# Optimization experiments

Measured on AMD Instinct MI355X. Metric: run time of the kernel, lower is better.

The kernel has to match this reference:

```python
import jax, jax.numpy as jnp
import numpy as np
from jax import lax

N_LAYER = 4
D_MODEL = 512
N_HEAD = 8
D_HEAD = 64
D_INNER = 2048
KERNEL = 9
POOL = 8
N_CLASSES = 10
BATCH = 4
RAW_LEN = 8192


def setup_inputs() -> dict:
    key = jax.random.key(0)
    ks = jax.random.split(key, 12)
    s = 0.02
    return {
        "signal": jax.random.normal(ks[0], (BATCH, RAW_LEN), jnp.float32),
        "conv_w": jax.random.normal(ks[1], (KERNEL, 1, D_MODEL), jnp.float32) * s,
        "conv_b": jnp.zeros((D_MODEL,), jnp.float32),
        "qkv_w": jax.random.normal(ks[2], (N_LAYER, D_MODEL, 3 * N_HEAD * D_HEAD), jnp.float32) * s,
        "r_w": jax.random.normal(ks[3], (N_LAYER, D_MODEL, N_HEAD * D_HEAD), jnp.float32) * s,
        "o_w": jax.random.normal(ks[4], (N_LAYER, N_HEAD * D_HEAD, D_MODEL), jnp.float32) * s,
        "ff1_w": jax.random.normal(ks[5], (N_LAYER, D_MODEL, D_INNER), jnp.float32) * s,
        "ff1_b": jnp.zeros((N_LAYER, D_INNER), jnp.float32),
        "ff2_w": jax.random.normal(ks[6], (N_LAYER, D_INNER, D_MODEL), jnp.float32) * s,
        "ff2_b": jnp.zeros((N_LAYER, D_MODEL), jnp.float32),
        "r_w_bias": jax.random.normal(ks[7], (N_HEAD, D_HEAD), jnp.float32) * s,
        "r_r_bias": jax.random.normal(ks[8], (N_HEAD, D_HEAD), jnp.float32) * s,
        "fc_w": jax.random.normal(ks[9], (D_MODEL, N_CLASSES), jnp.float32) * s,
        "fc_b": jnp.zeros((N_CLASSES,), jnp.float32),
    }


def _rel_shift(x):
    # x: [qlen, rlen, bsz, n_head]; TF-XL pad/reshape/slice trick
    q, r, b, n = x.shape
    x = jnp.pad(x, ((0, 0), (1, 0), (0, 0), (0, 0)))
    x = x.reshape(r + 1, q, b, n)[1:]
    return x.reshape(q, r, b, n)


def _forward(signal, conv_w, conv_b, qkv_w, r_w, o_w, ff1_w, ff1_b, ff2_w,
             ff2_b, r_w_bias, r_r_bias, fc_w, fc_b):
    # Conv1D (valid) -> ReLU -> AveragePooling1D
    x = signal[:, :, None]  # [B, L, 1]
    x = lax.conv_general_dilated(x, conv_w, (1,), 'VALID',
                                 dimension_numbers=('NWC', 'WIO', 'NWC')) + conv_b
    x = jax.nn.relu(x)
    B, Lp, D = x.shape
    S = Lp // POOL  # Lp is divisible by POOL for our sizes (keras valid pooling)
    x = x[:, :S * POOL].reshape(B, S, POOL, D).mean(axis=2)
    core = x.transpose(1, 0, 2)  # [S, B, D]

    # sinusoidal relative positional embedding, pos_seq = S-1 .. -(S-1)
    pos_seq = jnp.arange(S - 1, -S, -1, dtype=core.dtype)  # [2S-1]
    inv_freq = 1.0 / (10000.0 ** (jnp.arange(0, D, 2, dtype=core.dtype) / D))
    sin_inp = pos_seq[:, None] * inv_freq[None, :]
    pos_emb = jnp.concatenate([jnp.sin(sin_inp), jnp.cos(sin_inp)], -1)  # [2S-1, D]

    scale = 1.0 / np.sqrt(D_HEAD).astype(np.float32)
    for l in range(N_LAYER):
        heads = core @ qkv_w[l]  # [S, B, 3*H*Dh]
        q, k, v = jnp.split(heads, 3, axis=-1)
        q = q.reshape(S, B, N_HEAD, D_HEAD)
        k = k.reshape(S, B, N_HEAD, D_HEAD)
        v = v.reshape(S, B, N_HEAD, D_HEAD)
        rk = (pos_emb @ r_w[l]).reshape(2 * S - 1, N_HEAD, D_HEAD)

        AC = jnp.einsum('ibnd,jbnd->ijbn', q + r_w_bias, k)      # content term
        BD = jnp.einsum('ibnd,jnd->ijbn', q + r_r_bias, rk)      # position term
        BD = _rel_shift(BD)[:, :S]                                # [S, S, B, H]
        attn_prob = jax.nn.softmax((AC + BD) * scale, axis=1)
        attn_vec = jnp.einsum('ijbn,jbnd->ibnd', attn_prob, v)
        attn_out = attn_vec.reshape(S, B, N_HEAD * D_HEAD) @ o_w[l]
        core = core + attn_out

        # position-wise FF with residual
        h = jax.nn.relu(core @ ff1_w[l] + ff1_b[l]) @ ff2_w[l] + ff2_b[l]
        core = core + h

    # classification head on last timestep
    return core[-1] @ fc_w + fc_b  # [B, n_classes]


def reference(signal, conv_w, conv_b, qkv_w, r_w, o_w, ff1_w, ff1_b, ff2_w,
              ff2_b, r_w_bias, r_r_bias, fc_w, fc_b):
    return _forward(signal, conv_w, conv_b, qkv_w, r_w, o_w, ff1_w, ff1_b,
                    ff2_w, ff2_b, r_w_bias, r_r_bias, fc_w, fc_b)
```

## Files before the change

kernel.cpp:

```cpp
#include <hip/hip_runtime.h>
#include <math.h>

#define S_LEN   1023
#define BATCH_N 4
#define DMODEL  512
#define NHEAD   8
#define DHEAD   64
#define DINNER  2048
#define NLAYER  4
#define RAWLEN  8192
#define POOLW   8
#define KERNW   9
#define RLEN    (2*S_LEN-1)
#define MROWS   (S_LEN*BATCH_N)

using bf16x8 = __attribute__((ext_vector_type(8))) short;
using f32x4  = __attribute__((ext_vector_type(4))) float;

__device__ __forceinline__ unsigned short f2bf(float f) {
    union { float f; unsigned int u; } v; v.f = f;
    unsigned int u = v.u;
    return (unsigned short)((u + 0x7fffu + ((u >> 16) & 1u)) >> 16);
}
__device__ __forceinline__ float bf2f(unsigned short h) {
    union { unsigned int u; float f; } v; v.u = ((unsigned int)h) << 16;
    return v.f;
}

__device__ __forceinline__ void gload_lds16(const void* g, void* l) {
    using gvoid = const __attribute__((address_space(1))) void;
    using lvoid = __attribute__((address_space(3))) void;
    gvoid* gp = reinterpret_cast<gvoid*>(reinterpret_cast<unsigned long long>(g));
    lvoid* lp = reinterpret_cast<lvoid*>((unsigned int)reinterpret_cast<unsigned long long>(l));
    __builtin_amdgcn_global_load_lds(gp, lp, 16, 0, 0);
}

__global__ __launch_bounds__(512) void conv_pool_kernel(
    const float* __restrict__ sig, const float* __restrict__ cw,
    const float* __restrict__ cb, float* __restrict__ core,
    unsigned short* __restrict__ core_bf)
{
    int s = blockIdx.x, b = blockIdx.y, d = threadIdx.x;
    __shared__ float sseg[POOLW + KERNW - 1];
    if (d < POOLW + KERNW - 1) sseg[d] = sig[b*RAWLEN + s*POOLW + d];
    __syncthreads();
    float w[KERNW];
#pragma unroll
    for (int k = 0; k < KERNW; k++) w[k] = cw[k*DMODEL + d];
    float bias = cb[d];
    float acc = 0.f;
#pragma unroll
    for (int p = 0; p < POOLW; p++) {
        float c = bias;
#pragma unroll
        for (int k = 0; k < KERNW; k++) c = fmaf(sseg[p+k], w[k], c);
        acc += fmaxf(c, 0.f);
    }
    float v = acc * (1.0f/POOLW);
    core[(s*BATCH_N + b)*DMODEL + d] = v;
    core_bf[(s*BATCH_N + b)*DMODEL + d] = f2bf(v);
}

__global__ __launch_bounds__(512) void posemb_kernel(unsigned short* __restrict__ pe)
{
    int j = blockIdx.x, d = threadIdx.x;
    float pos = (float)(S_LEN - 1 - j);
    int i = (d < 256) ? d : d - 256;
    float invf = exp2f(-(float)i * (13.287712f/256.0f));
    float a = pos * invf;
    pe[j*DMODEL + d] = f2bf((d < 256) ? __sinf(a) : __cosf(a));
}

__global__ __launch_bounds__(256) void transpose_all_kernel(
    const float* __restrict__ qw, const float* __restrict__ rw,
    const float* __restrict__ ow, const float* __restrict__ f1,
    const float* __restrict__ f2,
    unsigned short* __restrict__ qT, unsigned short* __restrict__ rT,
    unsigned short* __restrict__ oT, unsigned short* __restrict__ f1T,
    unsigned short* __restrict__ f2T)
{
    int id = blockIdx.x;
    const float* W; unsigned short* Wt; int K, N, bx, by;
    if (id < 768)       { W = qw;  Wt = qT;  K = 512;  N = 1536; bx = id % 48; by = id / 48; }
    else if (id < 1024) { id -= 768;  W = rw;  Wt = rT;  K = 512;  N = 512;  bx = id % 16; by = id / 16; }
    else if (id < 1280) { id -= 1024; W = ow;  Wt = oT;  K = 512;  N = 512;  bx = id % 16; by = id / 16; }
    else if (id < 2304) { id -= 1280; W = f1;  Wt = f1T; K = 512;  N = 2048; bx = id % 64; by = id / 64; }
    else                { id -= 2304; W = f2;  Wt = f2T; K = 2048; N = 512;  bx = id % 16; by = id / 16; }

    __shared__ float L[32][33];
    int n0 = bx*32, k0 = by*32;
    int t = threadIdx.x;
    int kk = t>>3, nq = (t&7)*4;
    float4 v = *reinterpret_cast<const float4*>(&W[(size_t)(k0+kk)*N + n0 + nq]);
    L[kk][nq+0]=v.x; L[kk][nq+1]=v.y; L[kk][nq+2]=v.z; L[kk][nq+3]=v.w;
    __syncthreads();
    int nn = t>>3, kq = (t&7)*4;
    ushort4 o;
    o.x = f2bf(L[kq+0][nn]); o.y = f2bf(L[kq+1][nn]);
    o.z = f2bf(L[kq+2][nn]); o.w = f2bf(L[kq+3][nn]);
    *reinterpret_cast<ushort4*>(&Wt[(size_t)(n0+nn)*K + k0 + kq]) = o;
}

template<int BN, bool ACCUM, bool BIAS, bool RELU, bool WF32, bool WBF>
__device__ __forceinline__ void gemm_body(
    const unsigned short* __restrict__ A, const unsigned short* __restrict__ Bt,
    const float* __restrict__ bias, float* __restrict__ C,
    unsigned short* __restrict__ Cb, int M, int N, int K, int bm, int bn,
    unsigned short* As, unsigned short* Bs)
{
    constexpr int MF = (BN == 128) ? 4 : 2;
    int tid = threadIdx.x, lane = tid & 63, wid = tid >> 6;

    f32x4 acc[MF][4];
#pragma unroll
    for (int m=0;m<MF;m++)
#pragma unroll
        for (int n=0;n<4;n++) acc[m][n] = (f32x4){0.f,0.f,0.f,0.f};

    int r0 = wid*16 + (lane>>2);
    int slot = (lane&3)*8;
    int ga0 = bm + r0;      if (ga0 > M-1) ga0 = M-1;
    int ga1 = bm + r0 + 64; if (ga1 > M-1) ga1 = M-1;
    const unsigned short* pA0 = A  + (size_t)ga0*K + slot;
    const unsigned short* pA1 = A  + (size_t)ga1*K + slot;
    const unsigned short* pB0 = Bt + (size_t)(bn + r0)*K + slot;
    const unsigned short* pB1 = (BN==128) ? Bt + (size_t)(bn + r0 + 64)*K + slot : nullptr;
    char* lA0 = (char*)As + wid*1024;
    char* lA1 = (char*)As + (wid+4)*1024;
    char* lB0 = (char*)Bs + wid*1024;
    char* lB1 = (char*)Bs + (wid+4)*1024;

    int ar = (BN==128 ? (wid>>1)*64 : wid*32) + (lane&15);
    int br = (BN==128 ? (wid&1)*64 : 0) + (lane&15);
    int kc = (lane>>4)*8;

    for (int k0 = 0; k0 < K; k0 += 32) {
        __syncthreads();
        gload_lds16(pA0, lA0);
        gload_lds16(pA1, lA1);
        gload_lds16(pB0, lB0);
        if (BN == 128) gload_lds16(pB1, lB1);
        pA0 += 32; pA1 += 32; pB0 += 32; if (BN==128) pB1 += 32;
        __syncthreads();
        bf16x8 a[MF], b[4];
#pragma unroll
        for (int m=0;m<MF;m++) a[m] = *reinterpret_cast<const bf16x8*>(&As[(ar + m*16)*32 + kc]);
#pragma unroll
        for (int n=0;n<4;n++) b[n] = *reinterpret_cast<const bf16x8*>(&Bs[(br + n*16)*32 + kc]);
#pragma unroll
        for (int m=0;m<MF;m++)
#pragma unroll
            for (int n=0;n<4;n++)
                acc[m][n] = __builtin_amdgcn_mfma_f32_16x16x32_bf16(a[m], b[n], acc[m][n], 0,0,0);
    }

    int col0 = bn + (BN==128 ? (wid&1)*64 : 0) + (lane&15);
    int rbase = bm + (BN==128 ? (wid>>1)*64 : wid*32) + (lane>>4)*4;
#pragma unroll
    for (int m=0;m<MF;m++) {
#pragma unroll
        for (int n=0;n<4;n++) {
            int col = col0 + n*16;
            float bv = BIAS ? bias[col] : 0.f;
#pragma unroll
            for (int r=0;r<4;r++) {
                int row = rbase + m*16 + r;
                if (row < M) {
                    float v = acc[m][n][r] + bv;
                    if (RELU) v = fmaxf(v, 0.f);
                    size_t off = (size_t)row*N + col;
                    if (ACCUM) v += C[off];
                    if (WF32) C[off] = v;
                    if (WBF)  Cb[off] = f2bf(v);
                }
            }
        }
    }
}

template<int BN, bool ACCUM, bool BIAS, bool RELU, bool WF32, bool WBF>
__global__ __launch_bounds__(256) void gemm_mfma(
    const unsigned short* __restrict__ A, const unsigned short* __restrict__ Bt,
    const float* __restrict__ bias, float* __restrict__ C,
    unsigned short* __restrict__ Cb, int M, int N, int K)
{
    __shared__ unsigned short As[128*32];
    __shared__ unsigned short Bs[BN*32];
    gemm_body<BN,ACCUM,BIAS,RELU,WF32,WBF>(A, Bt, bias, C, Cb, M, N, K,
        blockIdx.y*128, blockIdx.x*BN, As, Bs);
}

__global__ __launch_bounds__(256) void gemm_qkvrk_kernel(
    const unsigned short* __restrict__ core_bf, const unsigned short* __restrict__ qkvT,
    unsigned short* __restrict__ heads,
    const unsigned short* __restrict__ pe_bf, const unsigned short* __restrict__ rwT,
    unsigned short* __restrict__ rk_bf)
{
    __shared__ unsigned short As[128*32];
    __shared__ unsigned short Bs[64*32];
    if (blockIdx.x < 24) {
        gemm_body<64,false,false,false,false,true>(core_bf, qkvT, nullptr, nullptr, heads,
            MROWS, 3*DMODEL, DMODEL, blockIdx.y*128, blockIdx.x*64, As, Bs);
    } else {
        if (blockIdx.y >= 16) return;
        gemm_body<64,false,false,false,false,true>(pe_bf, rwT, nullptr, nullptr, rk_bf,
            RLEN, DMODEL, DMODEL, blockIdx.y*128, (blockIdx.x-24)*64, As, Bs);
    }
}

template<bool ACCUM, bool BIAS, bool RELU, bool WF32, bool WBF>
__global__ __launch_bounds__(256) void gemm_mfma64(
    const unsigned short* __restrict__ A, const unsigned short* __restrict__ Bt,
    const float* __restrict__ bias, float* __restrict__ C,
    unsigned short* __restrict__ Cb, int M, int N, int K)
{
    __shared__ unsigned short As[64*32];
    __shared__ unsigned short Bs[64*32];
    int bm = blockIdx.y * 64, bn = blockIdx.x * 64;
    int tid = threadIdx.x, lane = tid & 63, wid = tid >> 6;
    int wr = wid >> 1, wc = wid & 1;

    f32x4 acc[2][2];
#pragma unroll
    for (int m=0;m<2;m++)
#pragma unroll
        for (int n=0;n<2;n++) acc[m][n] = (f32x4){0.f,0.f,0.f,0.f};

    int r0 = wid*16 + (lane>>2);
    int slot = (lane&3)*8;
    int ga = bm + r0; if (ga > M-1) ga = M-1;
    const unsigned short* pA = A  + (size_t)ga*K + slot;
    const unsigned short* pB = Bt + (size_t)(bn + r0)*K + slot;
    char* lA = (char*)As + wid*1024;
    char* lB = (char*)Bs + wid*1024;

    int ar = wr*32 + (lane&15);
    int br = wc*32 + (lane&15);
    int kc = (lane>>4)*8;

    for (int k0 = 0; k0 < K; k0 += 32) {
        __syncthreads();
        gload_lds16(pA, lA);
        gload_lds16(pB, lB);
        pA += 32; pB += 32;
        __syncthreads();
        bf16x8 a[2], b[2];
#pragma unroll
        for (int m=0;m<2;m++) a[m] = *reinterpret_cast<const bf16x8*>(&As[(ar + m*16)*32 + kc]);
#pragma unroll
        for (int n=0;n<2;n++) b[n] = *reinterpret_cast<const bf16x8*>(&Bs[(br + n*16)*32 + kc]);
#pragma unroll
        for (int m=0;m<2;m++)
#pragma unroll
            for (int n=0;n<2;n++)
                acc[m][n] = __builtin_amdgcn_mfma_f32_16x16x32_bf16(a[m], b[n], acc[m][n], 0,0,0);
    }

    int col0 = bn + wc*32 + (lane&15);
    int rbase = bm + wr*32 + (lane>>4)*4;
#pragma unroll
    for (int m=0;m<2;m++) {
#pragma unroll
        for (int n=0;n<2;n++) {
            int col = col0 + n*16;
            float bv = BIAS ? bias[col] : 0.f;
#pragma unroll
            for (int r=0;r<4;r++) {
                int row = rbase + m*16 + r;
                if (row < M) {
                    float v = acc[m][n][r] + bv;
                    if (RELU) v = fmaxf(v, 0.f);
                    size_t off = (size_t)row*N + col;
                    if (ACCUM) v += C[off];
                    if (WF32) C[off] = v;
                    if (WBF)  Cb[off] = f2bf(v);
                }
            }
        }
    }
}

#define TI 32
#define TJ 32
#define PSTR 40
#define ACSTR 36
#define BDSTR 68

__global__ __launch_bounds__(256) void attn_mfma_kernel(
    const unsigned short* __restrict__ heads,
    const unsigned short* __restrict__ rk,
    const float* __restrict__ rwb, const float* __restrict__ rrb,
    unsigned short* __restrict__ av)
{
    int i0 = blockIdx.x * TI;
    int bn = blockIdx.y; int b = bn >> 3, n = bn & 7;
    int tid = threadIdx.x, lane = tid & 63, wid = tid >> 6;
    int mi = wid >> 1;
    int half = wid & 1;
    int kc = (lane>>4)*8;
    int l15 = lane & 15;

    __shared__ float Sac[TI*ACSTR];
    __shared__ float Sbd[TI*BDSTR];
    __shared__ unsigned short Pb[TI*PSTR];
    __shared__ float mrow[TI], lrow[TI], frow[TI];

    const int base0 = (S_LEN-1) - i0 - (TI-1);

    bf16x8 qwf0, qwf1, qrf0, qrf1;
    {
        int gi = i0 + mi*16 + l15; if (gi > S_LEN-1) gi = S_LEN-1;
        const unsigned short* qb = heads + (size_t)(gi*BATCH_N + b)*1536 + n*64;
        bf16x8 u0 = *reinterpret_cast<const bf16x8*>(qb + kc);
        bf16x8 u1 = *reinterpret_cast<const bf16x8*>(qb + 32 + kc);
#pragma unroll
        for (int e=0;e<8;e++) {
            float f0 = bf2f((unsigned short)u0[e]);
            float f1 = bf2f((unsigned short)u1[e]);
            qwf0[e] = (short)f2bf(f0 + rwb[n*64 + kc + e]);
            qrf0[e] = (short)f2bf(f0 + rrb[n*64 + kc + e]);
            qwf1[e] = (short)f2bf(f1 + rwb[n*64 + 32 + kc + e]);
            qrf1[e] = (short)f2bf(f1 + rrb[n*64 + 32 + kc + e]);
        }
    }
    if (tid < TI) { mrow[tid] = -1e30f; lrow[tid] = 0.f; }

    f32x4 Oa[2];
    Oa[0] = (f32x4){0.f,0.f,0.f,0.f};
    Oa[1] = (f32x4){0.f,0.f,0.f,0.f};

    int rw = mi*16 + (lane>>4)*4;

    for (int t = 0; t < 32; t++) {
        int j0 = t * TJ;
        __syncthreads();

        {
            int gj = j0 + half*16 + l15; if (gj > S_LEN-1) gj = S_LEN-1;
            const unsigned short* kb = heads + (size_t)(gj*BATCH_N + b)*1536 + 512 + n*64;
            bf16x8 kf0 = *reinterpret_cast<const bf16x8*>(kb + kc);
            bf16x8 kf1 = *reinterpret_cast<const bf16x8*>(kb + 32 + kc);
            f32x4 s = (f32x4){0.f,0.f,0.f,0.f};
            s = __builtin_amdgcn_mfma_f32_16x16x32_bf16(qwf0, kf0, s, 0,0,0);
            s = __builtin_amdgcn_mfma_f32_16x16x32_bf16(qwf1, kf1, s, 0,0,0);
            int ci = half*16 + l15;
#pragma unroll
            for (int r=0;r<4;r++) Sac[(rw+r)*ACSTR + ci] = s[r];
        }
        if (t == 0) {
#pragma unroll
            for (int nn=0;nn<2;nn++) {
                int w = (half*2+nn)*16 + l15;
                int gr = base0 + w; gr = gr < 0 ? 0 : (gr > RLEN-1 ? RLEN-1 : gr);
                const unsigned short* rb = rk + (size_t)gr*DMODEL + n*64;
                bf16x8 rf0 = *reinterpret_cast<const bf16x8*>(rb + kc);
                bf16x8 rf1 = *reinterpret_cast<const bf16x8*>(rb + 32 + kc);
                f32x4 sb = (f32x4){0.f,0.f,0.f,0.f};
                sb = __builtin_amdgcn_mfma_f32_16x16x32_bf16(qrf0, rf0, sb, 0,0,0);
                sb = __builtin_amdgcn_mfma_f32_16x16x32_bf16(qrf1, rf1, sb, 0,0,0);
#pragma unroll
                for (int r=0;r<4;r++) Sbd[(rw+r)*BDSTR + w] = sb[r];
            }
        } else {
            int pblk = ((t & 1) ? 0 : 2) + half;
            int w = pblk*16 + l15;
            int off = 32*(t+1) + (w & 31);
            int gr = base0 + off; gr = gr < 0 ? 0 : (gr > RLEN-1 ? RLEN-1 : gr);
            const unsigned short* rb = rk + (size_t)gr*DMODEL + n*64;
            bf16x8 rf0 = *reinterpret_cast<const bf16x8*>(rb + kc);
            bf16x8 rf1 = *reinterpret_cast<const bf16x8*>(rb + 32 + kc);
            f32x4 sb = (f32x4){0.f,0.f,0.f,0.f};
            sb = __builtin_amdgcn_mfma_f32_16x16x32_bf16(qrf0, rf0, sb, 0,0,0);
            sb = __builtin_amdgcn_mfma_f32_16x16x32_bf16(qrf1, rf1, sb, 0,0,0);
#pragma unroll
            for (int r=0;r<4;r++) Sbd[(rw+r)*BDSTR + w] = sb[r];
        }
        __syncthreads();

        {
            int r = tid>>3, seg = tid&7, jl = seg*4;
            float4 ac = *reinterpret_cast<const float4*>(&Sac[r*ACSTR + jl]);
            int cbase = 32*t + (TI-1) - r;
            float s0 = (ac.x + Sbd[r*BDSTR + ((cbase+jl+0)&63)]) * 0.125f;
            float s1 = (ac.y + Sbd[r*BDSTR + ((cbase+jl+1)&63)]) * 0.125f;
            float s2 = (ac.z + Sbd[r*BDSTR + ((cbase+jl+2)&63)]) * 0.125f;
            float s3 = (ac.w + Sbd[r*BDSTR + ((cbase+jl+3)&63)]) * 0.125f;
            int jg = j0 + jl;
            if (jg+0 >= S_LEN) s0 = -1e30f;
            if (jg+1 >= S_LEN) s1 = -1e30f;
            if (jg+2 >= S_LEN) s2 = -1e30f;
            if (jg+3 >= S_LEN) s3 = -1e30f;
            float tm = fmaxf(fmaxf(s0,s1), fmaxf(s2,s3));
            tm = fmaxf(tm, __shfl_xor(tm, 1));
            tm = fmaxf(tm, __shfl_xor(tm, 2));
            tm = fmaxf(tm, __shfl_xor(tm, 4));
            float mo = mrow[r];
            float mnew = fmaxf(mo, tm);
            float f = __expf(mo - mnew);
            float e0 = __expf(s0 - mnew), e1 = __expf(s1 - mnew);
            float e2 = __expf(s2 - mnew), e3 = __expf(s3 - mnew);
            float ssum = e0+e1+e2+e3;
            ssum += __shfl_xor(ssum, 1);
            ssum += __shfl_xor(ssum, 2);
            ssum += __shfl_xor(ssum, 4);
            if (seg == 0) {
                mrow[r] = mnew;
                lrow[r] = lrow[r]*f + ssum;
                frow[r] = f;
            }
            ushort4 pw;
            pw.x = f2bf(e0); pw.y = f2bf(e1); pw.z = f2bf(e2); pw.w = f2bf(e3);
            *reinterpret_cast<ushort4*>(&Pb[r*PSTR + jl]) = pw;
        }
        __syncthreads();

        {
            float f0 = frow[rw+0], f1 = frow[rw+1], f2 = frow[rw+2], f3 = frow[rw+3];
#pragma unroll
            for (int nn=0;nn<2;nn++) {
                Oa[nn][0] *= f0; Oa[nn][1] *= f1; Oa[nn][2] *= f2; Oa[nn][3] *= f3;
            }
            bf16x8 pf = *reinterpret_cast<const bf16x8*>(&Pb[(mi*16 + l15)*PSTR + kc]);
            const unsigned short* vb = heads + 1024 + n*64;
#pragma unroll
            for (int nn=0;nn<2;nn++) {
                int d = (half*2+nn)*16 + l15;
                bf16x8 vf;
#pragma unroll
                for (int e=0;e<8;e++) {
                    int gj = j0 + kc + e; if (gj > S_LEN-1) gj = S_LEN-1;
                    vf[e] = (short)vb[(size_t)(gj*BATCH_N + b)*1536 + d];
                }
                Oa[nn] = __builtin_amdgcn_mfma_f32_16x16x32_bf16(pf, vf, Oa[nn], 0,0,0);
            }
        }
    }
    __syncthreads();

    {
        float linv[4];
#pragma unroll
        for (int r=0;r<4;r++) linv[r] = 1.0f / lrow[rw+r];
#pragma unroll
        for (int nn=0;nn<2;nn++) {
            int d = (half*2+nn)*16 + l15;
#pragma unroll
            for (int r=0;r<4;r++) {
                int gi = i0 + rw + r;
                if (gi < S_LEN)
                    av[(size_t)(gi*BATCH_N + b)*DMODEL + n*64 + d] = f2bf(Oa[nn][r]*linv[r]);
            }
        }
    }
}

__global__ __launch_bounds__(64) void final_kernel(
    const float* __restrict__ core, const float* __restrict__ fcw,
    const float* __restrict__ fcb, float* __restrict__ out)
{
    int idx = blockIdx.x;
    int b = idx / 10, c = idx % 10;
    int lane = threadIdx.x;
    const float* row = &core[(size_t)((S_LEN-1)*BATCH_N + b)*DMODEL];
    float acc = 0.f;
    for (int d = lane; d < DMODEL; d += 64)
        acc = fmaf(row[d], fcw[d*10 + c], acc);
#pragma unroll
    for (int off = 32; off; off >>= 1) acc += __shfl_xor(acc, off);
    if (lane == 0) out[b*10 + c] = acc + fcb[c];
}

extern "C" void kernel_launch(void* const* d_in, const int* in_sizes, int n_in,
                              void* d_out, int out_size, void* d_ws, size_t ws_size,
                              hipStream_t stream)
{
    const float* sig   = (const float*)d_in[0];
    const float* cw    = (const float*)d_in[1];
    const float* cb    = (const float*)d_in[2];
    const float* qkv_w = (const float*)d_in[3];
    const float* r_w   = (const float*)d_in[4];
    const float* o_w   = (const float*)d_in[5];
    const float* ff1_w = (const float*)d_in[6];
    const float* ff1_b = (const float*)d_in[7];
    const float* ff2_w = (const float*)d_in[8];
    const float* ff2_b = (const float*)d_in[9];
    const float* rwb   = (const float*)d_in[10];
    const float* rrb   = (const float*)d_in[11];
    const float* fcw   = (const float*)d_in[12];
    const float* fcb   = (const float*)d_in[13];
    float* out = (float*)d_out;

    float* core = (float*)d_ws;
    unsigned short* core_bf = (unsigned short*)(core + (size_t)MROWS*DMODEL);
    unsigned short* pe_bf   = core_bf + (size_t)MROWS*DMODEL;
    unsigned short* rk_bf   = pe_bf   + (size_t)RLEN*DMODEL;
    unsigned short* av_bf   = rk_bf   + (size_t)RLEN*DMODEL;
    unsigned short* big_bf  = av_bf   + (size_t)MROWS*DMODEL;
    unsigned short* qkvT = big_bf + (size_t)MROWS*DINNER;
    unsigned short* rwT  = qkvT + (size_t)(3*DMODEL)*DMODEL;
    unsigned short* owT  = rwT  + (size_t)DMODEL*DMODEL;
    unsigned short* ff1T = owT  + (size_t)DMODEL*DMODEL;
    unsigned short* ff2T = ff1T + (size_t)DINNER*DMODEL;

    conv_pool_kernel<<<dim3(S_LEN, BATCH_N), 512, 0, stream>>>(sig, cw, cb, core, core_bf);
    posemb_kernel<<<RLEN, 512, 0, stream>>>(pe_bf);

    for (int l = 0; l < NLAYER; l++) {
        transpose_all_kernel<<<3328, 256, 0, stream>>>(
            qkv_w + (size_t)l*DMODEL*(3*DMODEL),
            r_w   + (size_t)l*DMODEL*DMODEL,
            o_w   + (size_t)l*DMODEL*DMODEL,
            ff1_w + (size_t)l*DMODEL*DINNER,
            ff2_w + (size_t)l*DINNER*DMODEL,
            qkvT, rwT, owT, ff1T, ff2T);

        gemm_qkvrk_kernel<<<dim3(32,32), 256, 0, stream>>>(
            core_bf, qkvT, big_bf, pe_bf, rwT, rk_bf);
        attn_mfma_kernel<<<dim3(32,32), 256, 0, stream>>>(big_bf, rk_bf, rwb, rrb, av_bf);
        gemm_mfma64<true,false,false,true,true><<<dim3(8,64), 256, 0, stream>>>(
            av_bf, owT, nullptr, core, core_bf, MROWS, DMODEL, DMODEL);
        gemm_mfma<128,false,true,true,false,true><<<dim3(16,32), 256, 0, stream>>>(
            core_bf, ff1T, ff1_b + (size_t)l*DINNER, nullptr, big_bf, MROWS, DINNER, DMODEL);
        gemm_mfma64<true,true,false,true,true><<<dim3(8,64), 256, 0, stream>>>(
            big_bf, ff2T, ff2_b + (size_t)l*DMODEL, core, core_bf, MROWS, DMODEL, DINNER);
    }

    final_kernel<<<40, 64, 0, stream>>>(core, fcw, fcb, out);
}
```

Measured before the change: 702.3 us.

## Compute softmax in MFMA operand layout, dropping P shared buffer and barrier

Each wave now computes the online softmax directly for the rows and columns it feeds into the P·V MFMA, keeping the running max and sum in registers and producing the bf16 P operand without staging it. This removes the Pb shared buffer, the row-statistics arrays, one __syncthreads per tile and the final barrier. The cost is that both column-half waves of a row block redundantly compute the same softmax values, and rescale factors are moved with cross-lane shuffles.

```diff
diff --git a/kernel.cpp b/kernel.cpp
--- a/kernel.cpp
+++ b/kernel.cpp
@@ -282,7 +282,6 @@
 
 #define TI 32
 #define TJ 32
-#define PSTR 40
 #define ACSTR 36
 #define BDSTR 68
 
@@ -299,11 +298,10 @@
     int half = wid & 1;
     int kc = (lane>>4)*8;
     int l15 = lane & 15;
+    int rwl = (lane>>4)*4;
 
     __shared__ float Sac[TI*ACSTR];
     __shared__ float Sbd[TI*BDSTR];
-    __shared__ unsigned short Pb[TI*PSTR];
-    __shared__ float mrow[TI], lrow[TI], frow[TI];
 
     const int base0 = (S_LEN-1) - i0 - (TI-1);
 
@@ -323,13 +321,13 @@
             qrf1[e] = (short)f2bf(f1 + rrb[n*64 + 32 + kc + e]);
         }
     }
-    if (tid < TI) { mrow[tid] = -1e30f; lrow[tid] = 0.f; }
-
+
+    float mreg = -1e30f, lreg = 0.f;
     f32x4 Oa[2];
     Oa[0] = (f32x4){0.f,0.f,0.f,0.f};
     Oa[1] = (f32x4){0.f,0.f,0.f,0.f};
 
-    int rw = mi*16 + (lane>>4)*4;
+    int rw = mi*16 + rwl;
 
     for (int t = 0; t < 32; t++) {
         int j0 = t * TJ;
@@ -378,49 +376,44 @@
         __syncthreads();
 
         {
-            int r = tid>>3, seg = tid&7, jl = seg*4;
-            float4 ac = *reinterpret_cast<const float4*>(&Sac[r*ACSTR + jl]);
-            int cbase = 32*t + (TI-1) - r;
-            float s0 = (ac.x + Sbd[r*BDSTR + ((cbase+jl+0)&63)]) * 0.125f;
-            float s1 = (ac.y + Sbd[r*BDSTR + ((cbase+jl+1)&63)]) * 0.125f;
-            float s2 = (ac.z + Sbd[r*BDSTR + ((cbase+jl+2)&63)]) * 0.125f;
-            float s3 = (ac.w + Sbd[r*BDSTR + ((cbase+jl+3)&63)]) * 0.125f;
-            int jg = j0 + jl;
-            if (jg+0 >= S_LEN) s0 = -1e30f;
-            if (jg+1 >= S_LEN) s1 = -1e30f;
-            if (jg+2 >= S_LEN) s2 = -1e30f;
-            if (jg+3 >= S_LEN) s3 = -1e30f;
-            float tm = fmaxf(fmaxf(s0,s1), fmaxf(s2,s3));
-            tm = fmaxf(tm, __shfl_xor(tm, 1));
-            tm = fmaxf(tm, __shfl_xor(tm, 2));
-            tm = fmaxf(tm, __shfl_xor(tm, 4));
-            float mo = mrow[r];
-            float mnew = fmaxf(mo, tm);
-            float f = __expf(mo - mnew);
-            float e0 = __expf(s0 - mnew), e1 = __expf(s1 - mnew);
-            float e2 = __expf(s2 - mnew), e3 = __expf(s3 - mnew);
-            float ssum = e0+e1+e2+e3;
-            ssum += __shfl_xor(ssum, 1);
-            ssum += __shfl_xor(ssum, 2);
-            ssum += __shfl_xor(ssum, 4);
-            if (seg == 0) {
-                mrow[r] = mnew;
-                lrow[r] = lrow[r]*f + ssum;
-                frow[r] = f;
-            }
-            ushort4 pw;
-            pw.x = f2bf(e0); pw.y = f2bf(e1); pw.z = f2bf(e2); pw.w = f2bf(e3);
-            *reinterpret_cast<ushort4*>(&Pb[r*PSTR + jl]) = pw;
-        }
-        __syncthreads();
-
-        {
-            float f0 = frow[rw+0], f1 = frow[rw+1], f2 = frow[rw+2], f3 = frow[rw+3];
+            int prow = mi*16 + l15;
+            int cbase = 32*t + (TI-1) - prow;
+            float s[8];
+            float pmax = -1e30f;
+#pragma unroll
+            for (int e=0;e<8;e++) {
+                int col = kc + e;
+                float v = (Sac[prow*ACSTR + col] +
+                           Sbd[prow*BDSTR + ((cbase + col) & 63)]) * 0.125f;
+                if (j0 + col >= S_LEN) v = -1e30f;
+                s[e] = v;
+                pmax = fmaxf(pmax, v);
+            }
+            pmax = fmaxf(pmax, __shfl_xor(pmax, 16));
+            pmax = fmaxf(pmax, __shfl_xor(pmax, 32));
+            float mnew = fmaxf(mreg, pmax);
+            float fk = __expf(mreg - mnew);
+            bf16x8 pf;
+            float psum = 0.f;
+#pragma unroll
+            for (int e=0;e<8;e++) {
+                float p = __expf(s[e] - mnew);
+                psum += p;
+                pf[e] = (short)f2bf(p);
+            }
+            psum += __shfl_xor(psum, 16);
+            psum += __shfl_xor(psum, 32);
+            lreg = lreg*fk + psum;
+            mreg = mnew;
+
+            float fr0 = __shfl(fk, rwl + 0);
+            float fr1 = __shfl(fk, rwl + 1);
+            float fr2 = __shfl(fk, rwl + 2);
+            float fr3 = __shfl(fk, rwl + 3);
 #pragma unroll
             for (int nn=0;nn<2;nn++) {
-                Oa[nn][0] *= f0; Oa[nn][1] *= f1; Oa[nn][2] *= f2; Oa[nn][3] *= f3;
-            }
-            bf16x8 pf = *reinterpret_cast<const bf16x8*>(&Pb[(mi*16 + l15)*PSTR + kc]);
+                Oa[nn][0] *= fr0; Oa[nn][1] *= fr1; Oa[nn][2] *= fr2; Oa[nn][3] *= fr3;
+            }
             const unsigned short* vb = heads + 1024 + n*64;
 #pragma unroll
             for (int nn=0;nn<2;nn++) {
@@ -435,12 +428,11 @@
             }
         }
     }
-    __syncthreads();
 
     {
         float linv[4];
 #pragma unroll
-        for (int r=0;r<4;r++) linv[r] = 1.0f / lrow[rw+r];
+        for (int r=0;r<4;r++) linv[r] = 1.0f / __shfl(lreg, rwl + r);
 #pragma unroll
         for (int nn=0;nn<2;nn++) {
             int d = (half*2+nn)*16 + l15;
```

Result: slower. 725.5 us (+3.3%).
